# Kernel tuning notes

Measured on AMD Instinct MI355X. Metric: run time of the kernel, lower is better.

## Reference

```python
import jax, jax.numpy as jnp
import numpy as np

N = 128          # seed length cfg.n
EXTRA_RANDOM = 1 # cfg.extra_random_masks


def _make_masks(n: int, extra: int) -> np.ndarray:
    i = np.arange(n, dtype=np.int64)
    # Thue-Morse: parity of popcount(i)
    tm = np.array([bin(v).count('1') & 1 for v in i], dtype=np.uint8)
    # Sierpinski: row (n-1) of Pascal's triangle mod 2 (Lucas' theorem)
    sp = (((n - 1) & i) == i).astype(np.uint8)
    masks = [sp, tm]
    rng = np.random.default_rng(1234)
    for _ in range(extra):
        masks.append(rng.integers(0, 2, size=n, dtype=np.uint8))
    return np.stack(masks, axis=0)  # (K, n)


def setup_inputs() -> dict:
    key = jax.random.key(0)
    ks = jax.random.split(key, 8)
    B, n = 64, N
    T = n * (n + 1) // 2  # 8256
    H = 1024
    x = jax.random.randint(ks[0], (B, n), 0, 2, dtype=jnp.int32)
    masks = jnp.asarray(_make_masks(n, EXTRA_RANDOM))
    def lin(k, fan_in, fan_out):
        lim = 1.0 / np.sqrt(fan_in)
        return jax.random.uniform(k, (fan_in, fan_out), jnp.float32, -lim, lim)
    W0 = lin(ks[1], T, H); b0 = jnp.zeros((H,), jnp.float32)
    W1 = lin(ks[2], H, H); b1 = jnp.zeros((H,), jnp.float32)
    Wo = lin(ks[3], H, 1); bo = jnp.zeros((1,), jnp.float32)
    return {"x": x, "masks": masks, "W0": W0, "b0": b0,
            "W1": W1, "b1": b1, "Wo": Wo, "bo": bo}


def _features(x, masks):
    # x: (B, n) ints in {0,1}; masks: (K, n) uint8
    xb = x.astype(jnp.uint8)
    B, n = xb.shape
    # L3: dihedral orbit = n rotations + n rotations of the reversal -> 2n seeds
    idx = (jnp.arange(n)[:, None] + jnp.arange(n)[None, :]) % n  # (n, n)
    rot = xb[:, idx]                # (B, n, n)
    rev = xb[:, ::-1][:, idx]       # (B, n, n)
    seeds = jnp.concatenate([rot, rev], axis=1)  # (B, 2n, n)
    # L4: keep each seed plus XOR with each mask -> (1+K) variants per seed
    masked = jnp.bitwise_xor(seeds[:, :, None, :], masks[None, None, :, :])  # (B,2n,K,n)
    all_seeds = jnp.concatenate([seeds[:, :, None, :], masked], axis=2)
    M = all_seeds.shape[1] * all_seeds.shape[2]
    all_seeds = all_seeds.reshape(B, M, n)  # (B, M, n) uint8
    # XNOR triangle: row0 = seed, row_{k+1}[j] = xnor(row_k[j], row_k[j+1])
    rows = [all_seeds]
    cur = all_seeds
    for _ in range(n - 1):
        cur = 1 - jnp.bitwise_xor(cur[..., :-1], cur[..., 1:])
        rows.append(cur)
    feats = jnp.concatenate(rows, axis=-1)          # (B, M, T(n)) uint8
    f = jnp.mean(feats, axis=1, dtype=jnp.float32)  # mean pool over transforms
    return 2.0 * f - 1.0                            # {0,1} -> {-1,+1}


def reference(x, masks, W0, b0, W1, b1, Wo, bo):
    f = _features(x, masks)
    h = jax.nn.relu(f @ W0 + b0)
    h = jax.nn.relu(h @ W1 + b1)
    return h @ Wo + bo  # (B, 1) logits
```

## Files before the change

kernel.cpp:

```cpp
#include <hip/hip_runtime.h>
#include <cstdint>

#define DEVFN __device__ __forceinline__

struct U128 { unsigned long long lo, hi; };

DEVFN U128 rotr128(U128 w, int s) {
    U128 r;
    if (s == 64) { r.lo = w.hi; r.hi = w.lo; return r; }
    if (s < 64) {
        r.lo = (w.lo >> s) | (w.hi << (64 - s));
        r.hi = (w.hi >> s) | (w.lo << (64 - s));
    } else {
        int t = s - 64;
        unsigned long long lo = w.hi, hi = w.lo;
        r.lo = (lo >> t) | (hi << (64 - t));
        r.hi = (hi >> t) | (lo << (64 - t));
    }
    return r;
}

DEVFN U128 shr128(U128 w, int s) {
    U128 r;
    if (s == 64) { r.lo = w.hi; r.hi = 0ull; return r; }
    if (s < 64) {
        r.lo = (w.lo >> s) | (w.hi << (64 - s));
        r.hi = w.hi >> s;
    } else {
        r.lo = w.hi >> (s - 64); r.hi = 0ull;
    }
    return r;
}

__global__ __launch_bounds__(256) void kB(const int* __restrict__ x,
                                          const int* __restrict__ masks,
                                          const float* __restrict__ W0,
                                          float* __restrict__ Sm,
                                          float* __restrict__ G2) {
    int bid = blockIdx.x;
    int tid = threadIdx.x;

    if (bid == 768) {
        int b = tid >> 2;
        int rc = tid & 3;
        const int* xb = x + b * 128;
        U128 w; w.lo = 0ull; w.hi = 0ull;
        #pragma unroll
        for (int p = 0; p < 64; ++p) w.lo |= (unsigned long long)(xb[p] & 1) << p;
        #pragma unroll
        for (int p = 0; p < 64; ++p) w.hi |= (unsigned long long)(xb[64 + p] & 1) << p;
        int r0 = rc * 32;
        if (r0 & 32) { U128 t = rotr128(w, 32); w.lo ^= t.lo; w.hi ^= t.hi; }
        if (r0 & 64) { U128 t = rotr128(w, 64); w.lo ^= t.lo; w.hi ^= t.hi; }
        for (int rr = 0; rr < 32; ++rr) {
            int r = r0 + rr;
            int pc = __popcll(w.lo) + __popcll(w.hi);
            int sv = (r == 0) ? pc : (128 - pc);
            Sm[b * 128 + r] = (float)(2 * sv - 128);
            U128 t = rotr128(w, 1);
            w.lo ^= t.lo; w.hi ^= t.hi;
        }
        return;
    }

    int hc = bid & 3;
    int y  = bid >> 2;
    int r, jstart, jend, slice;
    if (y < 128) { r = y >> 1; slice = y & 1; jstart = slice * 64; jend = (slice == 0) ? 64 : (128 - r); }
    else         { r = y - 64;  slice = 0;    jstart = 0;          jend = 128 - r; }
    int L = jend - jstart;

    int lane = tid & 63;
    int g    = tid >> 6;

    __shared__ unsigned long long mw[3][2];
    __shared__ float cG[64];
    __shared__ float4 partG[4][64];

    if (tid < 128) {
        int half = tid >> 6;
        int lane_ = tid & 63;
        #pragma unroll
        for (int k = 0; k < 3; ++k) {
            unsigned long long bal = __ballot(masks[k * 128 + half * 64 + lane_] & 1);
            if (lane_ == 0) mw[k][half] = bal;
        }
    }
    __syncthreads();
    if (tid < 64) {
        int j = jstart + tid;
        int c = 0;
        #pragma unroll
        for (int k = 0; k < 3; ++k) {
            U128 m; m.lo = mw[k][0]; m.hi = mw[k][1];
            #pragma unroll
            for (int s = 1; s <= 64; s <<= 1) {
                if (r & s) { U128 t = shr128(m, s); m.lo ^= t.lo; m.hi ^= t.hi; }
            }
            int bit = (j < 64) ? (int)((m.lo >> j) & 1) : (int)((m.hi >> (j - 64)) & 1);
            c += bit;
        }
        cG[tid] = (float)(2 - c) * (1.0f / 256.0f);
    }
    __syncthreads();

    int off = r * 128 - (r * (r - 1)) / 2;
    const float* base = W0 + (size_t)(off + jstart) * 1024 + hc * 256 + lane * 4;
    float4 aG = {0.f, 0.f, 0.f, 0.f};
    #pragma unroll 4
    for (int jj = g; jj < L; jj += 4) {
        float4 v = *(const float4*)(base + (size_t)jj * 1024);
        float cg = cG[jj];
        aG.x += cg * v.x; aG.y += cg * v.y; aG.z += cg * v.z; aG.w += cg * v.w;
    }
    partG[g][lane] = aG;
    __syncthreads();

    if (tid < 64) {
        float4 sG = partG[0][tid];
        #pragma unroll
        for (int gg = 1; gg < 4; ++gg) {
            float4 pG = partG[gg][tid];
            sG.x += pG.x; sG.y += pG.y; sG.z += pG.z; sG.w += pG.w;
        }
        int row = slice * 128 + r;
        *(float4*)(G2 + (size_t)row * 1024 + hc * 256 + tid * 4) = sG;
    }
}

__global__ __launch_bounds__(256) void kF(const float* __restrict__ G2,
                                          const float* __restrict__ Sm,
                                          const float* __restrict__ b0,
                                          const float* __restrict__ W1,
                                          float* __restrict__ z1part) {
    int bid = blockIdx.x;
    int kc = bid & 15;
    int hc = (bid >> 4) & 7;
    int bs = bid >> 7;
    int tid = threadIdx.x;

    __shared__ float W1sh[64][128];
    __shared__ float Ssh[16][128];
    __shared__ float h0sh[16][64];

    #pragma unroll
    for (int t = 0; t < 32; ++t) {
        int idx = tid + t * 256;
        int kk = idx >> 7, hcl = idx & 127;
        W1sh[kk][hcl] = W1[(kc * 64 + kk) * 1024 + hc * 128 + hcl];
    }
    #pragma unroll
    for (int t = 0; t < 8; ++t) {
        int idx = tid + t * 256;
        int bl = idx >> 7, r = idx & 127;
        Ssh[bl][r] = Sm[(bs * 16 + bl) * 128 + r];
    }
    __syncthreads();

    {
        int k = tid & 63;
        int bg = tid >> 6;
        const float* g2p = G2 + kc * 64 + k;
        float acc[4] = {0.f, 0.f, 0.f, 0.f};
        #pragma unroll 8
        for (int row = 0; row < 192; ++row) {
            float gv = g2p[row * 1024];
            int r = row & 127;
            #pragma unroll
            for (int bb = 0; bb < 4; ++bb)
                acc[bb] += Ssh[bg * 4 + bb][r] * gv;
        }
        float base = b0[kc * 64 + k];
        #pragma unroll
        for (int bb = 0; bb < 4; ++bb)
            h0sh[bg * 4 + bb][k] = fmaxf(base + acc[bb], 0.f);
    }
    __syncthreads();

    {
        int hcol = tid & 127;
        int bg2 = tid >> 7;
        float acc2[8];
        #pragma unroll
        for (int i = 0; i < 8; ++i) acc2[i] = 0.f;
        #pragma unroll 4
        for (int kk = 0; kk < 64; ++kk) {
            float w = W1sh[kk][hcol];
            #pragma unroll
            for (int bb = 0; bb < 8; ++bb)
                acc2[bb] += h0sh[bg2 * 8 + bb][kk] * w;
        }
        #pragma unroll
        for (int bb = 0; bb < 8; ++bb) {
            int b = bs * 16 + bg2 * 8 + bb;
            z1part[(kc * 64 + b) * 1024 + hc * 128 + hcol] = acc2[bb];
        }
    }
}

__global__ __launch_bounds__(1024) void kE(const float* __restrict__ z1part,
                                           const float* __restrict__ b1,
                                           const float* __restrict__ Wo,
                                           const float* __restrict__ bo,
                                           float* __restrict__ out) {
    int b = blockIdx.x;
    int h = threadIdx.x;
    float z = b1[h];
    #pragma unroll
    for (int kc = 0; kc < 16; ++kc) z += z1part[(kc * 64 + b) * 1024 + h];
    float acc = fmaxf(z, 0.f) * Wo[h];
    #pragma unroll
    for (int off = 32; off >= 1; off >>= 1) acc += __shfl_down(acc, off);
    __shared__ float red[16];
    if ((h & 63) == 0) red[h >> 6] = acc;
    __syncthreads();
    if (h == 0) {
        float s = bo[0];
        #pragma unroll
        for (int i = 0; i < 16; ++i) s += red[i];
        out[b] = s;
    }
}

extern "C" void kernel_launch(void* const* d_in, const int* in_sizes, int n_in,
                              void* d_out, int out_size, void* d_ws, size_t ws_size,
                              hipStream_t stream) {
    const int*   x     = (const int*)d_in[0];
    const int*   masks = (const int*)d_in[1];
    const float* W0    = (const float*)d_in[2];
    const float* b0    = (const float*)d_in[3];
    const float* W1    = (const float*)d_in[4];
    const float* b1    = (const float*)d_in[5];
    const float* Wo    = (const float*)d_in[6];
    const float* bo    = (const float*)d_in[7];
    float* out = (float*)d_out;

    char* ws = (char*)d_ws;
    float* Sm     = (float*)(ws);
    float* G2     = (float*)(ws + (32u  << 10));
    float* z1part = (float*)(ws + (800u << 10));

    kB<<<769, 256, 0, stream>>>(x, masks, W0, Sm, G2);
    kF<<<512, 256, 0, stream>>>(G2, Sm, b0, W1, z1part);
    kE<<<64, 1024, 0, stream>>>(z1part, b1, Wo, bo, out);
}
```

Baseline: 33.73 us.

## Pair short and long triangle levels per block to balance W0 streaming work

```diff
diff --git a/kernel.cpp b/kernel.cpp
--- a/kernel.cpp
+++ b/kernel.cpp
@@ -32,15 +32,17 @@
     return r;
 }
 
+DEVFN int levoff(int r) { return r * 128 - (r * (r - 1)) / 2; }
+
 __global__ __launch_bounds__(256) void kB(const int* __restrict__ x,
                                           const int* __restrict__ masks,
                                           const float* __restrict__ W0,
                                           float* __restrict__ Sm,
-                                          float* __restrict__ G2) {
+                                          float* __restrict__ G3) {
     int bid = blockIdx.x;
     int tid = threadIdx.x;
 
-    if (bid == 768) {
+    if (bid == 512) {
         int b = tid >> 2;
         int rc = tid & 3;
         const int* xb = x + b * 128;
@@ -64,18 +66,21 @@
     }
 
     int hc = bid & 3;
-    int y  = bid >> 2;
-    int r, jstart, jend, slice;
-    if (y < 128) { r = y >> 1; slice = y & 1; jstart = slice * 64; jend = (slice == 0) ? 64 : (128 - r); }
-    else         { r = y - 64;  slice = 0;    jstart = 0;          jend = 128 - r; }
-    int L = jend - jstart;
+    int c2 = (bid >> 2) & 1;
+    int p  = bid >> 3;
+
+    int cntA = c2 ? (63 - p) : 65;
+    int cntB = c2 ? (p + 1)  : 0;
+    int L = cntA + cntB;
+    int jA0 = c2 ? 65 : 0;
 
     int lane = tid & 63;
     int g    = tid >> 6;
 
     __shared__ unsigned long long mw[3][2];
-    __shared__ float cG[64];
-    __shared__ float4 partG[4][64];
+    __shared__ float cG[65];
+    __shared__ float4 partG0[4][64];
+    __shared__ float4 partG1[4][64];
 
     if (tid < 128) {
         int half = tid >> 6;
@@ -87,8 +92,10 @@
         }
     }
     __syncthreads();
-    if (tid < 64) {
-        int j = jstart + tid;
+    if (tid < L) {
+        int r, j;
+        if (tid < cntA) { r = p;       j = jA0 + tid; }
+        else            { r = 127 - p; j = tid - cntA; }
         int c = 0;
         #pragma unroll
         for (int k = 0; k < 3; ++k) {
@@ -104,31 +111,39 @@
     }
     __syncthreads();
 
-    int off = r * 128 - (r * (r - 1)) / 2;
-    const float* base = W0 + (size_t)(off + jstart) * 1024 + hc * 256 + lane * 4;
-    float4 aG = {0.f, 0.f, 0.f, 0.f};
+    const float* baseA = W0 + (size_t)(levoff(p) + jA0) * 1024 + hc * 256 + lane * 4;
+    const float* baseB = W0 + (size_t)levoff(127 - p) * 1024 + hc * 256 + lane * 4;
+    float4 aG0 = {0.f, 0.f, 0.f, 0.f}, aG1 = {0.f, 0.f, 0.f, 0.f};
     #pragma unroll 4
     for (int jj = g; jj < L; jj += 4) {
-        float4 v = *(const float4*)(base + (size_t)jj * 1024);
+        bool inA = jj < cntA;
+        const float* addr = inA ? (baseA + (size_t)jj * 1024)
+                                : (baseB + (size_t)(jj - cntA) * 1024);
+        float4 v = *(const float4*)addr;
         float cg = cG[jj];
-        aG.x += cg * v.x; aG.y += cg * v.y; aG.z += cg * v.z; aG.w += cg * v.w;
-    }
-    partG[g][lane] = aG;
+        if (inA) { aG0.x += cg * v.x; aG0.y += cg * v.y; aG0.z += cg * v.z; aG0.w += cg * v.w; }
+        else     { aG1.x += cg * v.x; aG1.y += cg * v.y; aG1.z += cg * v.z; aG1.w += cg * v.w; }
+    }
+    partG0[g][lane] = aG0;
+    partG1[g][lane] = aG1;
     __syncthreads();
 
     if (tid < 64) {
-        float4 sG = partG[0][tid];
+        float4 s0 = partG0[0][tid], s1 = partG1[0][tid];
         #pragma unroll
         for (int gg = 1; gg < 4; ++gg) {
-            float4 pG = partG[gg][tid];
-            sG.x += pG.x; sG.y += pG.y; sG.z += pG.z; sG.w += pG.w;
-        }
-        int row = slice * 128 + r;
-        *(float4*)(G2 + (size_t)row * 1024 + hc * 256 + tid * 4) = sG;
-    }
-}
-
-__global__ __launch_bounds__(256) void kF(const float* __restrict__ G2,
+            float4 q0 = partG0[gg][tid], q1 = partG1[gg][tid];
+            s0.x += q0.x; s0.y += q0.y; s0.z += q0.z; s0.w += q0.w;
+            s1.x += q1.x; s1.y += q1.y; s1.z += q1.z; s1.w += q1.w;
+        }
+        int out0 = c2 ? (128 + p) : p;
+        *(float4*)(G3 + (size_t)out0 * 1024 + hc * 256 + tid * 4) = s0;
+        if (c2)
+            *(float4*)(G3 + (size_t)(64 + p) * 1024 + hc * 256 + tid * 4) = s1;
+    }
+}
+
+__global__ __launch_bounds__(256) void kF(const float* __restrict__ G3,
                                           const float* __restrict__ Sm,
                                           const float* __restrict__ b0,
                                           const float* __restrict__ W1,
@@ -160,12 +175,12 @@
     {
         int k = tid & 63;
         int bg = tid >> 6;
-        const float* g2p = G2 + kc * 64 + k;
+        const float* g2p = G3 + kc * 64 + k;
         float acc[4] = {0.f, 0.f, 0.f, 0.f};
         #pragma unroll 8
         for (int row = 0; row < 192; ++row) {
             float gv = g2p[row * 1024];
-            int r = row & 127;
+            int r = row < 64 ? row : (row < 128 ? 191 - row : row - 128);
             #pragma unroll
             for (int bb = 0; bb < 4; ++bb)
                 acc[bb] += Ssh[bg * 4 + bb][r] * gv;
@@ -193,7 +208,7 @@
         #pragma unroll
         for (int bb = 0; bb < 8; ++bb) {
             int b = bs * 16 + bg2 * 8 + bb;
-            z1part[(kc * 64 + b) * 1024 + hc * 128 + hcol] = acc2[bb];
+            z1part[((size_t)b * 16 + kc) * 1024 + hc * 128 + hcol] = acc2[bb];
         }
     }
 }
@@ -205,9 +220,10 @@
                                            float* __restrict__ out) {
     int b = blockIdx.x;
     int h = threadIdx.x;
+    const float* zp = z1part + (size_t)b * 16384 + h;
     float z = b1[h];
     #pragma unroll
-    for (int kc = 0; kc < 16; ++kc) z += z1part[(kc * 64 + b) * 1024 + h];
+    for (int kc = 0; kc < 16; ++kc) z += zp[kc * 1024];
     float acc = fmaxf(z, 0.f) * Wo[h];
     #pragma unroll
     for (int off = 32; off >= 1; off >>= 1) acc += __shfl_down(acc, off);
@@ -237,10 +253,10 @@
 
     char* ws = (char*)d_ws;
     float* Sm     = (float*)(ws);
-    float* G2     = (float*)(ws + (32u  << 10));
+    float* G3     = (float*)(ws + (32u  << 10));
     float* z1part = (float*)(ws + (800u << 10));
 
-    kB<<<769, 256, 0, stream>>>(x, masks, W0, Sm, G2);
-    kF<<<512, 256, 0, stream>>>(G2, Sm, b0, W1, z1part);
+    kB<<<513, 256, 0, stream>>>(x, masks, W0, Sm, G3);
+    kF<<<512, 256, 0, stream>>>(G3, Sm, b0, W1, z1part);
     kE<<<64, 1024, 0, stream>>>(z1part, b1, Wo, bo, out);
 }
```

Result: slower. 34.84 us (+3.3%).

## Fuse final reduction kernel into kF via last-block atomic counters

Applied to the files above, without the earlier changes.

```diff
diff --git a/kernel.cpp b/kernel.cpp
--- a/kernel.cpp
+++ b/kernel.cpp
@@ -36,11 +36,14 @@
                                           const int* __restrict__ masks,
                                           const float* __restrict__ W0,
                                           float* __restrict__ Sm,
-                                          float* __restrict__ G2) {
+                                          float* __restrict__ G2,
+                                          int* __restrict__ cnt) {
     int bid = blockIdx.x;
     int tid = threadIdx.x;
 
     if (bid == 768) {
+        if (tid < 36)
+            __hip_atomic_store(&cnt[tid], 0, __ATOMIC_RELAXED, __HIP_MEMORY_SCOPE_AGENT);
         int b = tid >> 2;
         int rc = tid & 3;
         const int* xb = x + b * 128;
@@ -128,20 +131,29 @@
     }
 }
 
-__global__ __launch_bounds__(256) void kF(const float* __restrict__ G2,
-                                          const float* __restrict__ Sm,
-                                          const float* __restrict__ b0,
-                                          const float* __restrict__ W1,
-                                          float* __restrict__ z1part) {
+__global__ __launch_bounds__(256) void kFE(const float* __restrict__ G2,
+                                           const float* __restrict__ Sm,
+                                           const float* __restrict__ b0,
+                                           const float* __restrict__ W1,
+                                           const float* __restrict__ b1,
+                                           const float* __restrict__ Wo,
+                                           const float* __restrict__ bo,
+                                           float* __restrict__ z1part,
+                                           float* __restrict__ outpart,
+                                           int* __restrict__ cnt,
+                                           float* __restrict__ out) {
     int bid = blockIdx.x;
-    int kc = bid & 15;
-    int hc = (bid >> 4) & 7;
-    int bs = bid >> 7;
+    int G  = bid & 31;
+    int kc = bid >> 5;
+    int hc = G >> 2;
+    int bs = G & 3;
     int tid = threadIdx.x;
 
     __shared__ float W1sh[64][128];
     __shared__ float Ssh[16][128];
     __shared__ float h0sh[16][64];
+    __shared__ float wredLDS[4][4];
+    __shared__ int lastFlag;
 
     #pragma unroll
     for (int t = 0; t < 32; ++t) {
@@ -192,33 +204,62 @@
         }
         #pragma unroll
         for (int bb = 0; bb < 8; ++bb) {
-            int b = bs * 16 + bg2 * 8 + bb;
-            z1part[(kc * 64 + b) * 1024 + hc * 128 + hcol] = acc2[bb];
-        }
-    }
-}
-
-__global__ __launch_bounds__(1024) void kE(const float* __restrict__ z1part,
-                                           const float* __restrict__ b1,
-                                           const float* __restrict__ Wo,
-                                           const float* __restrict__ bo,
-                                           float* __restrict__ out) {
-    int b = blockIdx.x;
-    int h = threadIdx.x;
-    float z = b1[h];
-    #pragma unroll
-    for (int kc = 0; kc < 16; ++kc) z += z1part[(kc * 64 + b) * 1024 + h];
-    float acc = fmaxf(z, 0.f) * Wo[h];
-    #pragma unroll
-    for (int off = 32; off >= 1; off >>= 1) acc += __shfl_down(acc, off);
-    __shared__ float red[16];
-    if ((h & 63) == 0) red[h >> 6] = acc;
-    __syncthreads();
-    if (h == 0) {
+            int bl = bg2 * 8 + bb;
+            z1part[((size_t)(G * 16 + kc) * 16 + bl) * 128 + hcol] = acc2[bb];
+        }
+    }
+
+    asm volatile("s_waitcnt vmcnt(0)" ::: "memory");
+    __syncthreads();
+    if (tid == 0) {
+        int old = atomicAdd(&cnt[G], 1);
+        lastFlag = (old == 15);
+    }
+    __syncthreads();
+    if (!lastFlag) return;
+
+    {
+        int w = tid >> 6, l = tid & 63;
+        float2 wo2 = *(const float2*)&Wo[hc * 128 + 2 * l];
+        float2 b12 = *(const float2*)&b1[hc * 128 + 2 * l];
+        const float* zb = z1part + (size_t)G * 16 * 2048;
+        #pragma unroll
+        for (int p = 0; p < 4; ++p) {
+            int bl = p * 4 + w;
+            float zx = b12.x, zy = b12.y;
+            #pragma unroll
+            for (int kc2 = 0; kc2 < 16; ++kc2) {
+                float2 v = *(const float2*)&zb[(kc2 * 16 + bl) * 128 + 2 * l];
+                zx += v.x; zy += v.y;
+            }
+            float val = fmaxf(zx, 0.f) * wo2.x + fmaxf(zy, 0.f) * wo2.y;
+            #pragma unroll
+            for (int off = 32; off >= 1; off >>= 1) val += __shfl_down(val, off);
+            if (l == 0) wredLDS[p][w] = val;
+        }
+    }
+    __syncthreads();
+    if (tid < 16)
+        __hip_atomic_store(&outpart[(bs * 8 + hc) * 16 + tid],
+                           wredLDS[tid >> 2][tid & 3],
+                           __ATOMIC_RELAXED, __HIP_MEMORY_SCOPE_AGENT);
+    asm volatile("s_waitcnt vmcnt(0)" ::: "memory");
+    __syncthreads();
+
+    if (tid == 0) {
+        int old2 = atomicAdd(&cnt[32 + bs], 1);
+        lastFlag = (old2 == 7);
+    }
+    __syncthreads();
+    if (!lastFlag) return;
+
+    if (tid < 16) {
         float s = bo[0];
         #pragma unroll
-        for (int i = 0; i < 16; ++i) s += red[i];
-        out[b] = s;
+        for (int hc2 = 0; hc2 < 8; ++hc2)
+            s += __hip_atomic_load(&outpart[(bs * 8 + hc2) * 16 + tid],
+                                   __ATOMIC_RELAXED, __HIP_MEMORY_SCOPE_AGENT);
+        out[bs * 16 + tid] = s;
     }
 }
 
@@ -236,11 +277,13 @@
     float* out = (float*)d_out;
 
     char* ws = (char*)d_ws;
-    float* Sm     = (float*)(ws);
-    float* G2     = (float*)(ws + (32u  << 10));
-    float* z1part = (float*)(ws + (800u << 10));
-
-    kB<<<769, 256, 0, stream>>>(x, masks, W0, Sm, G2);
-    kF<<<512, 256, 0, stream>>>(G2, Sm, b0, W1, z1part);
-    kE<<<64, 1024, 0, stream>>>(z1part, b1, Wo, bo, out);
-}
+    float* Sm      = (float*)(ws);
+    float* G2      = (float*)(ws + (32u   << 10));
+    float* z1part  = (float*)(ws + (800u  << 10));
+    float* outpart = (float*)(ws + (4896u << 10));
+    int*   cnt     = (int*)  (ws + (4898u << 10));
+
+    kB<<<769, 256, 0, stream>>>(x, masks, W0, Sm, G2, cnt);
+    kFE<<<512, 256, 0, stream>>>(G2, Sm, b0, W1, b1, Wo, bo,
+                                 z1part, outpart, cnt, out);
+}
```

After: 39.16 us. +16.1%, slower.
